# Optimization experiments

Hardware: AMD Instinct MI355X
Metric: run time of the kernel (lower is better)

## Reference

```python
import jax, jax.numpy as jnp
import numpy as np

LMBDA = 0.1
ALPHA = 0.05
NBIT = 4


def setup_inputs() -> dict:
    key = jax.random.key(0)
    k1, k2 = jax.random.split(key)
    shape = (4096, 16384)
    weight = jax.random.normal(k1, shape, dtype=jnp.float32) * 0.05
    Qn, Qp = -2 ** (NBIT - 1), 2 ** (NBIT - 1) - 1
    q_int = jax.random.randint(k2, shape, Qn, Qp + 1)  # bins in [-8, 7]
    weight_q = (q_int.astype(jnp.float32)) * ALPHA
    alpha = jnp.full((1,), ALPHA, dtype=jnp.float32)
    return {"weight": weight, "weight_q": weight_q, "nbit": NBIT, "alpha": alpha}


def reference(weight, weight_q, nbit, alpha):
    # dampening_loss with aggregation='mean', scaled by lmbda (single quant layer)
    Qn = -2 ** (nbit - 1)
    Qp = 2 ** (nbit - 1) - 1
    nbins = Qp - Qn + 1
    a = alpha.reshape(())

    # (w_q.detach() - w)^2 mean  (detach is a no-op in fwd)
    loss = jnp.mean((weight_q - weight) ** 2)

    # Fused histogram pass: per-bin count / sum / sumsq of `weight`,
    # keyed by the quant bin of weight_q (exact-equality mask in original).
    bin_id = jnp.round(weight_q / a).astype(jnp.int32) - Qn  # [0, nbins)
    w = weight.reshape(-1)
    b = bin_id.reshape(-1)
    cnt = jax.ops.segment_sum(jnp.ones_like(w), b, num_segments=nbins)
    s = jax.ops.segment_sum(w, b, num_segments=nbins)
    ss = jax.ops.segment_sum(w * w, b, num_segments=nbins)

    # unbiased variance per bin, only added when count > 1 (as in torch.var)
    denom_n = jnp.maximum(cnt, 1.0)
    denom_nm1 = jnp.maximum(cnt - 1.0, 1.0)
    var = (ss - s * s / denom_n) / denom_nm1
    loss = loss + jnp.sum(jnp.where(cnt > 1.0, var, 0.0))

    return LMBDA * loss
```

## Files before the change

kernel.cpp:

```cpp
#include <hip/hip_runtime.h>

#define NBINS  16
#define TPB    256
#define BLOCKS 1024
#define DUMMY  16
#define MAGIC  12582912.0f


__global__ __launch_bounds__(TPB, 4) void binreg_main(
    const float* __restrict__ w, const float* __restrict__ wq,
    const float* __restrict__ alpha_p, const int* __restrict__ nbit_p,
    float* __restrict__ partial, long long n)
{
    __shared__ float2 sv_pl[(NBINS + 1) * TPB];
    __shared__ float  cred[NBINS][TPB / 64];
    __shared__ float  sqpart[TPB / 64];

    const int tid = threadIdx.x;

    #pragma unroll
    for (int k = 0; k < NBINS; ++k)
        sv_pl[k * TPB + tid] = make_float2(0.0f, 0.0f);

    const float inv_a = 1.0f / alpha_p[0];
    const int   qoff  = 1 << (nbit_p[0] - 1);

    const long long n4     = n >> 2;
    const long long stride = (long long)BLOCKS * TPB;
    const float4* w4 = (const float4*)w;
    const float4* q4 = (const float4*)wq;

    float sq = 0.0f;
    unsigned long long clo = 0ull, chi = 0ull;
    float cf[NBINS];
    #pragma unroll
    for (int k = 0; k < NBINS; ++k) cf[k] = 0.0f;
    int pend = 0;

    auto process = [&](float4 a, float4 b) {
        float d0 = b.x - a.x, d1 = b.y - a.y, d2 = b.z - a.z, d3 = b.w - a.w;
        sq += d0 * d0 + d1 * d1 + d2 * d2 + d3 * d3;

        const int b0 = (__float_as_int(fmaf(b.x, inv_a, MAGIC)) + qoff) & (NBINS - 1);
        const int b1 = (__float_as_int(fmaf(b.y, inv_a, MAGIC)) + qoff) & (NBINS - 1);
        const int b2 = (__float_as_int(fmaf(b.z, inv_a, MAGIC)) + qoff) & (NBINS - 1);
        const int b3 = (__float_as_int(fmaf(b.w, inv_a, MAGIC)) + qoff) & (NBINS - 1);

        {
            unsigned long long t;
            t = 1ull << ((b0 & 7) << 3); clo += (b0 < 8) ? t : 0ull; chi += (b0 < 8) ? 0ull : t;
            t = 1ull << ((b1 & 7) << 3); clo += (b1 < 8) ? t : 0ull; chi += (b1 < 8) ? 0ull : t;
            t = 1ull << ((b2 & 7) << 3); clo += (b2 < 8) ? t : 0ull; chi += (b2 < 8) ? 0ull : t;
            t = 1ull << ((b3 & 7) << 3); clo += (b3 < 8) ? t : 0ull; chi += (b3 < 8) ? 0ull : t;
        }

        const bool e10 = (b1 == b0);
        const bool e20 = (b2 == b0);
        const bool e21 = (b2 == b1) && !e20;
        const bool e30 = (b3 == b0);
        const bool e31 = (b3 == b1) && !e30;
        const bool e32 = (b3 == b2) && !e30 && !e31;

        float sx0 = a.x, sx1 = a.y, sx2 = a.z, sx3 = a.w;
        float qx0 = a.x * a.x, qx1 = a.y * a.y, qx2 = a.z * a.z, qx3 = a.w * a.w;

        sx0 += e10 ? sx1 : 0.0f;  qx0 += e10 ? qx1 : 0.0f;
        sx0 += e20 ? sx2 : 0.0f;  qx0 += e20 ? qx2 : 0.0f;
        sx1 += e21 ? sx2 : 0.0f;  qx1 += e21 ? qx2 : 0.0f;
        sx0 += e30 ? sx3 : 0.0f;  qx0 += e30 ? qx3 : 0.0f;
        sx1 += e31 ? sx3 : 0.0f;  qx1 += e31 ? qx3 : 0.0f;
        sx2 += e32 ? sx3 : 0.0f;  qx2 += e32 ? qx3 : 0.0f;

        const int r1 = e10               ? DUMMY : b1;
        const int r2 = (e20 | e21)       ? DUMMY : b2;
        const int r3 = (e30 | e31 | e32) ? DUMMY : b3;
        const int a0 = (b0 << 8) + tid;
        const int a1 = (r1 << 8) + tid;
        const int a2 = (r2 << 8) + tid;
        const int a3 = (r3 << 8) + tid;

        float2 t0 = sv_pl[a0];
        float2 t1 = sv_pl[a1];
        float2 t2 = sv_pl[a2];
        float2 t3 = sv_pl[a3];
        t0.x += sx0; t0.y += qx0;
        t1.x += sx1; t1.y += qx1;
        t2.x += sx2; t2.y += qx2;
        t3.x += sx3; t3.y += qx3;
        sv_pl[a0] = t0;
        sv_pl[a1] = t1;
        sv_pl[a2] = t2;
        sv_pl[a3] = t3;
    };

    const long long start = (long long)blockIdx.x * TPB + tid;
    long long cnt = 0;
    if (start < n4) cnt = 1 + (n4 - 1 - start) / stride;

    const float4* pw = w4 + start;
    const float4* pq = q4 + start;

    float4 aw0, aq0, aw1, aq1;
    if (cnt >= 1) { aw0 = pw[0];      aq0 = pq[0]; }
    if (cnt >= 2) { aw1 = pw[stride]; aq1 = pq[stride]; }

    long long k = 0;
    while (k + 3 < cnt) {
        float4 nw0 = pw[2 * stride], nq0 = pq[2 * stride];
        process(aw0, aq0);
        float4 nw1 = pw[3 * stride], nq1 = pq[3 * stride];
        process(aw1, aq1);
        aw0 = nw0; aq0 = nq0; aw1 = nw1; aq1 = nq1;
        pw += 2 * stride; pq += 2 * stride;
        k += 2;

        if (++pend >= 16) {
            #pragma unroll
            for (int kk = 0; kk < 8; ++kk) {
                cf[kk]     += (float)((clo >> (kk * 8)) & 0xffull);
                cf[kk + 8] += (float)((chi >> (kk * 8)) & 0xffull);
            }
            clo = 0ull; chi = 0ull; pend = 0;
        }
    }
    {
        const long long rem = cnt - k;
        if (rem == 3) {
            float4 nw = pw[2 * stride], nq = pq[2 * stride];
            process(aw0, aq0); process(aw1, aq1); process(nw, nq);
        } else if (rem == 2) {
            process(aw0, aq0); process(aw1, aq1);
        } else if (rem == 1) {
            process(aw0, aq0);
        }
    }

    for (long long t = (n4 << 2) + start; t < n; t += stride) {
        float av = w[t], bv = wq[t];
        float d = bv - av;
        sq += d * d;
        int bb = (__float_as_int(fmaf(bv, inv_a, MAGIC)) + qoff) & (NBINS - 1);
        unsigned long long one = 1ull << ((bb & 7) << 3);
        clo += (bb < 8) ? one : 0ull; chi += (bb < 8) ? 0ull : one;
        int aa = (bb << 8) + tid;
        float2 tt = sv_pl[aa]; tt.x += av; tt.y += av * av; sv_pl[aa] = tt;
    }

    #pragma unroll
    for (int kk = 0; kk < 8; ++kk) {
        cf[kk]     += (float)((clo >> (kk * 8)) & 0xffull);
        cf[kk + 8] += (float)((chi >> (kk * 8)) & 0xffull);
    }

    for (int off = 32; off; off >>= 1) sq += __shfl_down(sq, off, 64);
    const int wave = tid >> 6, lane = tid & 63;
    if (lane == 0) sqpart[wave] = sq;

    #pragma unroll
    for (int kk = 0; kk < NBINS; ++kk) {
        float v = cf[kk];
        for (int off = 32; off; off >>= 1) v += __shfl_down(v, off, 64);
        if (lane == 0) cred[kk][wave] = v;
    }
    __syncthreads();

    if (tid < NBINS)
        partial[tid * BLOCKS + blockIdx.x] =
            cred[tid][0] + cred[tid][1] + cred[tid][2] + cred[tid][3];

    for (int c = 16 + wave; c < 48; c += 4) {
        const int bin = c & 15;
        float v = 0.0f;
        if (c < 32) {
            #pragma unroll
            for (int r = 0; r < TPB / 64; ++r)
                v += sv_pl[(bin << 8) + r * 64 + lane].x;
        } else {
            #pragma unroll
            for (int r = 0; r < TPB / 64; ++r)
                v += sv_pl[(bin << 8) + r * 64 + lane].y;
        }
        for (int off = 32; off; off >>= 1) v += __shfl_down(v, off, 64);
        if (lane == 0) partial[c * BLOCKS + blockIdx.x] = v;
    }
    if (tid == 0)
        partial[48 * BLOCKS + blockIdx.x] =
            sqpart[0] + sqpart[1] + sqpart[2] + sqpart[3];
}

__global__ __launch_bounds__(TPB) void binreg_final(
    const float* __restrict__ partial, float* __restrict__ out, long long n)
{
    __shared__ float cell[49];
    const int tid = threadIdx.x, wave = tid >> 6, lane = tid & 63;

    for (int c = wave; c < 49; c += 4) {
        float v0 = 0.0f, v1 = 0.0f, v2 = 0.0f, v3 = 0.0f;
        for (int r = lane; r < BLOCKS; r += 256) {
            v0 += partial[c * BLOCKS + r];
            v1 += partial[c * BLOCKS + r + 64];
            v2 += partial[c * BLOCKS + r + 128];
            v3 += partial[c * BLOCKS + r + 192];
        }
        float v = (v0 + v1) + (v2 + v3);
        for (int off = 32; off; off >>= 1) v += __shfl_down(v, off, 64);
        if (lane == 0) cell[c] = v;
    }
    __syncthreads();

    if (tid == 0) {
        float loss = cell[48] / (float)n;
        #pragma unroll
        for (int b = 0; b < NBINS; ++b) {
            float cnt = cell[b];
            float s   = cell[16 + b];
            float ss  = cell[32 + b];
            if (cnt > 1.0f)
                loss += (ss - s * s / cnt) / (cnt - 1.0f);
        }
        out[0] = 0.1f * loss;
    }
}

extern "C" void kernel_launch(void* const* d_in, const int* in_sizes, int n_in,
                              void* d_out, int out_size, void* d_ws, size_t ws_size,
                              hipStream_t stream)
{
    const float* w     = (const float*)d_in[0];
    const float* wq    = (const float*)d_in[1];
    const int*   nbit  = (const int*)d_in[2];
    const float* alpha = (const float*)d_in[3];
    float* out     = (float*)d_out;
    float* partial = (float*)d_ws;
    long long n = (long long)in_sizes[0];

    binreg_main<<<BLOCKS, TPB, 0, stream>>>(w, wq, alpha, nbit, partial, n);
    binreg_final<<<1, TPB, 0, stream>>>(partial, out, n);
}
```

Baseline: 532.0 us.

## Stream inputs through a 4-deep async global-to-LDS pipeline

Replaces the register double-buffered float4 loads with `global_load_lds` direct-to-LDS transfers into a 4-stage ring buffer for both weight and weight_q. Explicit `s_waitcnt vmcnt` waits keep up to three stages in flight while the current stage is processed. The goal is to hide memory latency in a kernel that is reading well below peak bandwidth. In exchange, LDS use per block roughly doubles and launch bounds drop from 4 to 2 blocks, so occupancy falls; a generic fallback loop handles non-uniform sizes.

```diff
diff --git a/kernel.cpp b/kernel.cpp
--- a/kernel.cpp
+++ b/kernel.cpp
@@ -3,20 +3,33 @@
 #define NBINS  16
 #define TPB    256
 #define BLOCKS 1024
+#define DEPTH  4
 #define DUMMY  16
 #define MAGIC  12582912.0f
 
 
-__global__ __launch_bounds__(TPB, 4) void binreg_main(
+typedef unsigned long long u64;
+
+__device__ __forceinline__ void gload_lds16(const void* g, void* l)
+{
+    __builtin_amdgcn_global_load_lds(
+        (const __attribute__((address_space(1))) unsigned int*)g,
+        (__attribute__((address_space(3))) unsigned int*)l, 16, 0, 0);
+}
+
+__global__ __launch_bounds__(TPB, 2) void binreg_main(
     const float* __restrict__ w, const float* __restrict__ wq,
     const float* __restrict__ alpha_p, const int* __restrict__ nbit_p,
     float* __restrict__ partial, long long n)
 {
     __shared__ float2 sv_pl[(NBINS + 1) * TPB];
+    __shared__ float4 stgW[DEPTH][TPB];
+    __shared__ float4 stgQ[DEPTH][TPB];
     __shared__ float  cred[NBINS][TPB / 64];
     __shared__ float  sqpart[TPB / 64];
 
-    const int tid = threadIdx.x;
+    const int tid    = threadIdx.x;
+    const int wvbase = tid & ~63;
 
     #pragma unroll
     for (int k = 0; k < NBINS; ++k)
@@ -31,11 +44,19 @@
     const float4* q4 = (const float4*)wq;
 
     float sq = 0.0f;
-    unsigned long long clo = 0ull, chi = 0ull;
+    u64 clo = 0ull, chi = 0ull;
     float cf[NBINS];
     #pragma unroll
     for (int k = 0; k < NBINS; ++k) cf[k] = 0.0f;
-    int pend = 0;
+
+    #define FLUSH_COUNTS() do {                                   \
+        _Pragma("unroll")                                         \
+        for (int kk_ = 0; kk_ < 8; ++kk_) {                       \
+            cf[kk_]     += (float)((clo >> (kk_ * 8)) & 0xffull); \
+            cf[kk_ + 8] += (float)((chi >> (kk_ * 8)) & 0xffull); \
+        }                                                         \
+        clo = 0ull; chi = 0ull;                                   \
+    } while (0)
 
     auto process = [&](float4 a, float4 b) {
         float d0 = b.x - a.x, d1 = b.y - a.y, d2 = b.z - a.z, d3 = b.w - a.w;
@@ -47,7 +68,7 @@
         const int b3 = (__float_as_int(fmaf(b.w, inv_a, MAGIC)) + qoff) & (NBINS - 1);
 
         {
-            unsigned long long t;
+            u64 t;
             t = 1ull << ((b0 & 7) << 3); clo += (b0 < 8) ? t : 0ull; chi += (b0 < 8) ? 0ull : t;
             t = 1ull << ((b1 & 7) << 3); clo += (b1 < 8) ? t : 0ull; chi += (b1 < 8) ? 0ull : t;
             t = 1ull << ((b2 & 7) << 3); clo += (b2 < 8) ? t : 0ull; chi += (b2 < 8) ? 0ull : t;
@@ -94,63 +115,64 @@
     };
 
     const long long start = (long long)blockIdx.x * TPB + tid;
-    long long cnt = 0;
-    if (start < n4) cnt = 1 + (n4 - 1 - start) / stride;
-
-    const float4* pw = w4 + start;
-    const float4* pq = q4 + start;
-
-    float4 aw0, aq0, aw1, aq1;
-    if (cnt >= 1) { aw0 = pw[0];      aq0 = pq[0]; }
-    if (cnt >= 2) { aw1 = pw[stride]; aq1 = pq[stride]; }
-
-    long long k = 0;
-    while (k + 3 < cnt) {
-        float4 nw0 = pw[2 * stride], nq0 = pq[2 * stride];
-        process(aw0, aq0);
-        float4 nw1 = pw[3 * stride], nq1 = pq[3 * stride];
-        process(aw1, aq1);
-        aw0 = nw0; aq0 = nq0; aw1 = nw1; aq1 = nq1;
-        pw += 2 * stride; pq += 2 * stride;
-        k += 2;
-
-        if (++pend >= 16) {
-            #pragma unroll
-            for (int kk = 0; kk < 8; ++kk) {
-                cf[kk]     += (float)((clo >> (kk * 8)) & 0xffull);
-                cf[kk + 8] += (float)((chi >> (kk * 8)) & 0xffull);
-            }
-            clo = 0ull; chi = 0ull; pend = 0;
-        }
-    }
-    {
-        const long long rem = cnt - k;
-        if (rem == 3) {
-            float4 nw = pw[2 * stride], nq = pq[2 * stride];
-            process(aw0, aq0); process(aw1, aq1); process(nw, nq);
-        } else if (rem == 2) {
-            process(aw0, aq0); process(aw1, aq1);
-        } else if (rem == 1) {
-            process(aw0, aq0);
-        }
-    }
-
-    for (long long t = (n4 << 2) + start; t < n; t += stride) {
+    const long long tail_begin = n4 << 2;
+
+    const bool uniform = (n4 > 0) && (n4 % stride == 0);
+    const int  C       = uniform ? (int)(n4 / stride) : 0;
+
+    if (uniform && C >= DEPTH) {
+        const float4* pw = w4 + start;
+        const float4* pq = q4 + start;
+
+        #define ISSUE(J) do {                                              \
+            gload_lds16(pw + (long long)(J) * stride,                      \
+                        &stgW[(J) & (DEPTH - 1)][wvbase]);                 \
+            gload_lds16(pq + (long long)(J) * stride,                      \
+                        &stgQ[(J) & (DEPTH - 1)][wvbase]);                 \
+        } while (0)
+
+        ISSUE(0); ISSUE(1); ISSUE(2);
+
+        int pend = 0;
+        #pragma unroll 1
+        for (int k = 0; k + DEPTH <= C; ++k) {
+            ISSUE(k + 3);
+            asm volatile("s_waitcnt vmcnt(6)" ::: "memory");
+            float4 a = stgW[k & (DEPTH - 1)][tid];
+            float4 b = stgQ[k & (DEPTH - 1)][tid];
+            process(a, b);
+            if (++pend >= 32) { FLUSH_COUNTS(); pend = 0; }
+        }
+        FLUSH_COUNTS();
+        {
+            int k = C - 3;
+            asm volatile("s_waitcnt vmcnt(4)" ::: "memory");
+            process(stgW[k & (DEPTH - 1)][tid], stgQ[k & (DEPTH - 1)][tid]); ++k;
+            asm volatile("s_waitcnt vmcnt(2)" ::: "memory");
+            process(stgW[k & (DEPTH - 1)][tid], stgQ[k & (DEPTH - 1)][tid]); ++k;
+            asm volatile("s_waitcnt vmcnt(0)" ::: "memory");
+            process(stgW[k & (DEPTH - 1)][tid], stgQ[k & (DEPTH - 1)][tid]);
+        }
+        #undef ISSUE
+    } else if (n4 > 0) {
+        int pend = 0;
+        for (long long i = start; i < n4; i += stride) {
+            process(w4[i], q4[i]);
+            if (++pend >= 32) { FLUSH_COUNTS(); pend = 0; }
+        }
+    }
+
+    for (long long t = tail_begin + start; t < n; t += stride) {
         float av = w[t], bv = wq[t];
         float d = bv - av;
         sq += d * d;
         int bb = (__float_as_int(fmaf(bv, inv_a, MAGIC)) + qoff) & (NBINS - 1);
-        unsigned long long one = 1ull << ((bb & 7) << 3);
+        u64 one = 1ull << ((bb & 7) << 3);
         clo += (bb < 8) ? one : 0ull; chi += (bb < 8) ? 0ull : one;
         int aa = (bb << 8) + tid;
         float2 tt = sv_pl[aa]; tt.x += av; tt.y += av * av; sv_pl[aa] = tt;
     }
-
-    #pragma unroll
-    for (int kk = 0; kk < 8; ++kk) {
-        cf[kk]     += (float)((clo >> (kk * 8)) & 0xffull);
-        cf[kk + 8] += (float)((chi >> (kk * 8)) & 0xffull);
-    }
+    FLUSH_COUNTS();
 
     for (int off = 32; off; off >>= 1) sq += __shfl_down(sq, off, 64);
     const int wave = tid >> 6, lane = tid & 63;
```

Measured after the change: 551.7 us. 3.7% more time.
